# Optimization experiments

Hardware: AMD Instinct MI355X
Metric: run time of the kernel (lower is better)

The kernel has to match this reference:

```python
import jax, jax.numpy as jnp
import numpy as np

P0 = 2   # tublet_size
P = 16   # patch_size
FC = 2   # flow channels (map_x, map_y)


def patchify(x, p0, p1, p2):
    # x: (B, C, T, H, W) -> (B, (T/p0)(H/p1)(W/p2), p0*p1*p2*C)
    B, C, T, H, W = x.shape
    x = x.reshape(B, C, T // p0, p0, H // p1, p1, W // p2, p2)
    x = x.transpose(0, 2, 4, 6, 3, 5, 7, 1)  # b t h w p0 p1 p2 c
    return x.reshape(B, (T // p0) * (H // p1) * (W // p2), p0 * p1 * p2 * C)


def unpatchify(x, p0, p1, p2, C, T, H, W):
    # x: (B, N, p0*p1*p2*C) -> (B, C, T, H, W)
    B = x.shape[0]
    x = x.reshape(B, T // p0, H // p1, W // p2, p0, p1, p2, C)
    x = x.transpose(0, 7, 1, 4, 2, 5, 3, 6)  # b c t p0 h p1 w p2
    return x.reshape(B, C, T, H, W)


def bilinear_warp(imgs, mx, my):
    # imgs: (B, C, T, H, W); mx, my: (B, T, H, W) absolute sample coords.
    # Equivalent of cv2.remap INTER_LINEAR with constant (zero) border.
    B, C, T, H, W = imgs.shape
    x0 = jnp.floor(mx)
    y0 = jnp.floor(my)
    wx = (mx - x0).reshape(B, 1, T, H * W)
    wy = (my - y0).reshape(B, 1, T, H * W)
    x0i = x0.astype(jnp.int32)
    y0i = y0.astype(jnp.int32)
    imgs_flat = imgs.reshape(B, C, T, H * W)

    def gather(yi, xi):
        yc = jnp.clip(yi, 0, H - 1)
        xc = jnp.clip(xi, 0, W - 1)
        idx = (yc * W + xc).reshape(B, 1, T, H * W)
        v = jnp.take_along_axis(imgs_flat, jnp.broadcast_to(idx, (B, C, T, H * W)), axis=-1)
        valid = ((yi >= 0) & (yi <= H - 1) & (xi >= 0) & (xi <= W - 1)).reshape(B, 1, T, H * W)
        return v * valid.astype(v.dtype)

    v00 = gather(y0i, x0i)
    v01 = gather(y0i, x0i + 1)
    v10 = gather(y0i + 1, x0i)
    v11 = gather(y0i + 1, x0i + 1)
    out = (v00 * (1 - wx) * (1 - wy) + v01 * wx * (1 - wy)
           + v10 * (1 - wx) * wy + v11 * wx * wy)
    return out.reshape(B, C, T, H, W)


def setup_inputs() -> dict:
    key = jax.random.key(0)
    k1, k2, k3 = jax.random.split(key, 3)
    B, C, T, H, W = 8, 3, 16, 224, 224
    N = (T // P0) * (H // P) * (W // P)         # 1568 tokens
    D = P0 * P * P * FC                         # 1024 per-token flow dim
    output = jax.random.normal(k1, (B, N, D), dtype=jnp.float32)
    raw_target = jax.random.normal(k2, (B, C, T, H, W), dtype=jnp.float32)
    mask = jax.random.randint(k3, (B, N), 0, 2) > 0
    return {"output": output, "raw_target": raw_target, "mask": mask}


def reference(output, raw_target, mask):
    B, C, T, H, W = raw_target.shape
    # tokens -> dense flow field (B, 2, T, H, W)
    flows = unpatchify(output, P0, P, P, FC, T, H, W)
    gx = jnp.arange(W, dtype=flows.dtype)               # (W,)
    gy = jnp.arange(H, dtype=flows.dtype)[:, None]      # (H, 1)
    mx = flows[:, 0] + gx                                # (B, T, H, W)
    my = flows[:, 1] + gy
    recons = bilinear_warp(raw_target, mx, my)           # (B, C, T, H, W)
    rec_p = patchify(recons, P0, P, P)                   # (B, N, p0*p1*p2*C)
    tgt_p = patchify(raw_target, P0, P, P)
    m = mask.astype(rec_p.dtype)[..., None]              # (B, N, 1)
    diff2 = (rec_p - tgt_p) ** 2 * m
    denom = jnp.maximum(m.sum(), 1.0) * rec_p.shape[-1]
    return diff2.sum() / denom
```

## Files before the change

kernel.cpp:

```cpp
#include <hip/hip_runtime.h>

#define Bd 8
#define Cd 3
#define Td 16
#define Hd 224
#define Wd 224
#define Nd 1568
#define HWd (Hd*Wd)
#define NTOK (Bd*Nd)
#define GRID_MAIN (NTOK*2)
#define PATCH_ELEMS 1536.0

__global__ __launch_bounds__(256, 8)
void flow_mse_gather(const float* __restrict__ outp,
                     const float* __restrict__ raw,
                     const int* __restrict__ mask,
                     float* __restrict__ partial) {
    const int tid = threadIdx.x;
    const int bid = blockIdx.x;
    const int ft  = bid >> 1;
    const int i0  = bid & 1;

    if (mask[ft] == 0) {
        if (tid == 0) partial[bid] = 0.f;
        return;
    }

    const int b  = ft / Nd;
    const int n  = ft - b * Nd;
    const int t2 = n / 196;
    const int rm = n - t2 * 196;
    const int ph = rm / 14;
    const int pw = rm - ph * 14;
    const int t  = (t2 << 1) | i0;

    const int py = tid >> 4, px = tid & 15;
    const int h  = (ph << 4) + py;
    const int w  = (pw << 4) + px;

    const float2 f = ((const float2*)(outp + ((size_t)ft << 10) + (i0 << 9)))[tid];

    const float mx = f.x + (float)w;
    const float my = f.y + (float)h;
    const float x0 = floorf(mx), y0 = floorf(my);
    const float wx = mx - x0,    wy = my - y0;
    const int x0i = (int)x0, y0i = (int)y0;
    const int x1i = x0i + 1,  y1i = y0i + 1;

    const bool vx0 = (x0i >= 0) && (x0i < Wd);
    const bool vx1 = (x1i >= 0) && (x1i < Wd);
    const bool vy0 = (y0i >= 0) && (y0i < Hd);
    const bool vy1 = (y1i >= 0) && (y1i < Hd);

    const float W00 = (1.f - wx) * (1.f - wy) * ((vx0 && vy0) ? 1.f : 0.f);
    const float W01 = wx         * (1.f - wy) * ((vx1 && vy0) ? 1.f : 0.f);
    const float W10 = (1.f - wx) * wy         * ((vx0 && vy1) ? 1.f : 0.f);
    const float W11 = wx         * wy         * ((vx1 && vy1) ? 1.f : 0.f);

    const int xc0 = min(max(x0i, 0), Wd - 1);
    const int xc1 = min(max(x1i, 0), Wd - 1);
    const int yc0 = min(max(y0i, 0), Hd - 1);
    const int yc1 = min(max(y1i, 0), Hd - 1);

    const int i00 = yc0 * Wd + xc0;
    const int i01 = yc0 * Wd + xc1;
    const int i10 = yc1 * Wd + xc0;
    const int i11 = yc1 * Wd + xc1;
    const int itg = h * Wd + w;

    const float* base = raw + (size_t)(b * (Cd * Td) + t) * HWd;
    float acc = 0.f;
    #pragma unroll
    for (int c = 0; c < Cd; ++c) {
        const float* img = base + (size_t)c * (Td * HWd);
        float rec = img[i00] * W00 + img[i01] * W01
                  + img[i10] * W10 + img[i11] * W11;
        float d = rec - img[itg];
        acc += d * d;
    }

    __shared__ float sred[4];
    for (int off = 32; off > 0; off >>= 1) acc += __shfl_down(acc, off, 64);
    if ((tid & 63) == 0) sred[tid >> 6] = acc;
    __syncthreads();
    if (tid == 0) partial[bid] = sred[0] + sred[1] + sred[2] + sred[3];
}

__global__ void finalize_kernel(const float* __restrict__ partial,
                                const int* __restrict__ mask,
                                float* __restrict__ out) {
    const int tid = threadIdx.x;
    double s = 0.0;
    for (int i = tid; i < GRID_MAIN; i += 256) s += (double)partial[i];
    int c = 0;
    for (int i = tid; i < NTOK; i += 256) c += (mask[i] != 0) ? 1 : 0;
    for (int off = 32; off > 0; off >>= 1) {
        s += __shfl_down(s, off, 64);
        c += __shfl_down(c, off, 64);
    }
    __shared__ double sd[4];
    __shared__ int    sc[4];
    int lane = tid & 63, wid = tid >> 6;
    if (lane == 0) { sd[wid] = s; sc[wid] = c; }
    __syncthreads();
    if (tid == 0) {
        double st = sd[0] + sd[1] + sd[2] + sd[3];
        int    ct = sc[0] + sc[1] + sc[2] + sc[3];
        double denom = (double)(ct > 0 ? ct : 1) * PATCH_ELEMS;
        out[0] = (float)(st / denom);
    }
}

extern "C" void kernel_launch(void* const* d_in, const int* in_sizes, int n_in,
                              void* d_out, int out_size, void* d_ws, size_t ws_size,
                              hipStream_t stream) {
    const float* outp = (const float*)d_in[0];
    const float* raw  = (const float*)d_in[1];
    const int*   mask = (const int*)d_in[2];
    float* out = (float*)d_out;

    float* partial = (float*)d_ws;

    flow_mse_gather<<<GRID_MAIN, 256, 0, stream>>>(outp, raw, mask, partial);
    finalize_kernel<<<1, 256, 0, stream>>>(partial, mask, out);
}
```

Before: 190.5 us.

## Compact masked tokens into a list and process both frames per block

A new compaction kernel ballot-scans the mask into a per-segment list of active token indices. The main kernel launches one block per token, and blocks past the active count exit at once, so masked-out tokens no longer occupy blocks that do a mask load before exiting. Each block now handles both temporal frames of a token. Partial sums are combined with a float atomicAdd, which replaces the double-precision finalize pass over partials but makes the summation order nondeterministic and less precise.

```diff
diff --git a/kernel.cpp b/kernel.cpp
--- a/kernel.cpp
+++ b/kernel.cpp
@@ -8,106 +8,154 @@
 #define Nd 1568
 #define HWd (Hd*Wd)
 #define NTOK (Bd*Nd)
-#define GRID_MAIN (NTOK*2)
+#define GRID_MAIN NTOK
+#define NSEG 13
 #define PATCH_ELEMS 1536.0
 
-__global__ __launch_bounds__(256, 8)
+__global__ void compact_kernel(const int* __restrict__ mask,
+                               int* __restrict__ list,
+                               int* __restrict__ bcnt,
+                               float* __restrict__ acc) {
+    const int j   = blockIdx.x;
+    const int tid = threadIdx.x;
+    const int i   = (j << 10) + tid;
+    if (j == 0 && tid == 0) acc[0] = 0.f;
+    bool m = (i < NTOK) && (mask[i] != 0);
+    unsigned long long bal = __ballot(m);
+    int lane = tid & 63, wid = tid >> 6;
+    __shared__ unsigned wt[16];
+    unsigned pre = (unsigned)__popcll(bal & ((1ull << lane) - 1ull));
+    if (lane == 0) wt[wid] = (unsigned)__popcll(bal);
+    __syncthreads();
+    unsigned base = 0;
+    for (int k = 0; k < wid; ++k) base += wt[k];
+    if (m) list[(j << 10) + base + pre] = i;
+    if (tid == 0) {
+        unsigned tot = 0;
+        #pragma unroll
+        for (int k = 0; k < 16; ++k) tot += wt[k];
+        bcnt[j] = (int)tot;
+    }
+}
+
+__global__ __launch_bounds__(256, 6)
 void flow_mse_gather(const float* __restrict__ outp,
                      const float* __restrict__ raw,
-                     const int* __restrict__ mask,
-                     float* __restrict__ partial) {
+                     const int* __restrict__ list,
+                     const int* __restrict__ bcnt,
+                     float* __restrict__ acc) {
     const int tid = threadIdx.x;
     const int bid = blockIdx.x;
-    const int ft  = bid >> 1;
-    const int i0  = bid & 1;
 
-    if (mask[ft] == 0) {
-        if (tid == 0) partial[bid] = 0.f;
-        return;
-    }
+    int pre1  = bcnt[0];
+    int pre2  = pre1  + bcnt[1];
+    int pre3  = pre2  + bcnt[2];
+    int pre4  = pre3  + bcnt[3];
+    int pre5  = pre4  + bcnt[4];
+    int pre6  = pre5  + bcnt[5];
+    int pre7  = pre6  + bcnt[6];
+    int pre8  = pre7  + bcnt[7];
+    int pre9  = pre8  + bcnt[8];
+    int pre10 = pre9  + bcnt[9];
+    int pre11 = pre10 + bcnt[10];
+    int pre12 = pre11 + bcnt[11];
+    const int cnt = pre12 + bcnt[12];
+    if (bid >= cnt) return;
 
-    const int b  = ft / Nd;
-    const int n  = ft - b * Nd;
+    int seg = 0, sbase = 0;
+    if (bid >= pre1)  { seg = 1;  sbase = pre1;  }
+    if (bid >= pre2)  { seg = 2;  sbase = pre2;  }
+    if (bid >= pre3)  { seg = 3;  sbase = pre3;  }
+    if (bid >= pre4)  { seg = 4;  sbase = pre4;  }
+    if (bid >= pre5)  { seg = 5;  sbase = pre5;  }
+    if (bid >= pre6)  { seg = 6;  sbase = pre6;  }
+    if (bid >= pre7)  { seg = 7;  sbase = pre7;  }
+    if (bid >= pre8)  { seg = 8;  sbase = pre8;  }
+    if (bid >= pre9)  { seg = 9;  sbase = pre9;  }
+    if (bid >= pre10) { seg = 10; sbase = pre10; }
+    if (bid >= pre11) { seg = 11; sbase = pre11; }
+    if (bid >= pre12) { seg = 12; sbase = pre12; }
+    const int tk = list[(seg << 10) + bid - sbase];
+
+    const int b  = tk / Nd;
+    const int n  = tk - b * Nd;
     const int t2 = n / 196;
     const int rm = n - t2 * 196;
     const int ph = rm / 14;
     const int pw = rm - ph * 14;
-    const int t  = (t2 << 1) | i0;
 
     const int py = tid >> 4, px = tid & 15;
     const int h  = (ph << 4) + py;
     const int w  = (pw << 4) + px;
-
-    const float2 f = ((const float2*)(outp + ((size_t)ft << 10) + (i0 << 9)))[tid];
-
-    const float mx = f.x + (float)w;
-    const float my = f.y + (float)h;
-    const float x0 = floorf(mx), y0 = floorf(my);
-    const float wx = mx - x0,    wy = my - y0;
-    const int x0i = (int)x0, y0i = (int)y0;
-    const int x1i = x0i + 1,  y1i = y0i + 1;
-
-    const bool vx0 = (x0i >= 0) && (x0i < Wd);
-    const bool vx1 = (x1i >= 0) && (x1i < Wd);
-    const bool vy0 = (y0i >= 0) && (y0i < Hd);
-    const bool vy1 = (y1i >= 0) && (y1i < Hd);
-
-    const float W00 = (1.f - wx) * (1.f - wy) * ((vx0 && vy0) ? 1.f : 0.f);
-    const float W01 = wx         * (1.f - wy) * ((vx1 && vy0) ? 1.f : 0.f);
-    const float W10 = (1.f - wx) * wy         * ((vx0 && vy1) ? 1.f : 0.f);
-    const float W11 = wx         * wy         * ((vx1 && vy1) ? 1.f : 0.f);
-
-    const int xc0 = min(max(x0i, 0), Wd - 1);
-    const int xc1 = min(max(x1i, 0), Wd - 1);
-    const int yc0 = min(max(y0i, 0), Hd - 1);
-    const int yc1 = min(max(y1i, 0), Hd - 1);
-
-    const int i00 = yc0 * Wd + xc0;
-    const int i01 = yc0 * Wd + xc1;
-    const int i10 = yc1 * Wd + xc0;
-    const int i11 = yc1 * Wd + xc1;
     const int itg = h * Wd + w;
 
-    const float* base = raw + (size_t)(b * (Cd * Td) + t) * HWd;
-    float acc = 0.f;
+    const float* frow = outp + ((size_t)tk << 10);
+    float2 f0 = ((const float2*)frow)[tid];
+    float2 f1 = ((const float2*)(frow + 512))[tid];
+
+    float Wt[2][4];
+    int   tp[2][4];
+    #pragma unroll
+    for (int s = 0; s < 2; ++s) {
+        float2 f = s ? f1 : f0;
+        float mx = f.x + (float)w;
+        float my = f.y + (float)h;
+        float x0 = floorf(mx), y0 = floorf(my);
+        float wx = mx - x0,    wy = my - y0;
+        int x0i = (int)x0, y0i = (int)y0;
+        int x1i = x0i + 1,  y1i = y0i + 1;
+
+        bool vx0 = (x0i >= 0) && (x0i < Wd);
+        bool vx1 = (x1i >= 0) && (x1i < Wd);
+        bool vy0 = (y0i >= 0) && (y0i < Hd);
+        bool vy1 = (y1i >= 0) && (y1i < Hd);
+
+        Wt[s][0] = (1.f - wx) * (1.f - wy) * ((vx0 && vy0) ? 1.f : 0.f);
+        Wt[s][1] = wx         * (1.f - wy) * ((vx1 && vy0) ? 1.f : 0.f);
+        Wt[s][2] = (1.f - wx) * wy         * ((vx0 && vy1) ? 1.f : 0.f);
+        Wt[s][3] = wx         * wy         * ((vx1 && vy1) ? 1.f : 0.f);
+
+        int xc0 = min(max(x0i, 0), Wd - 1);
+        int xc1 = min(max(x1i, 0), Wd - 1);
+        int yc0 = min(max(y0i, 0), Hd - 1);
+        int yc1 = min(max(y1i, 0), Hd - 1);
+        tp[s][0] = yc0 * Wd + xc0;
+        tp[s][1] = yc0 * Wd + xc1;
+        tp[s][2] = yc1 * Wd + xc0;
+        tp[s][3] = yc1 * Wd + xc1;
+    }
+
+    float a = 0.f;
     #pragma unroll
     for (int c = 0; c < Cd; ++c) {
-        const float* img = base + (size_t)c * (Td * HWd);
-        float rec = img[i00] * W00 + img[i01] * W01
-                  + img[i10] * W10 + img[i11] * W11;
-        float d = rec - img[itg];
-        acc += d * d;
+        #pragma unroll
+        for (int s = 0; s < 2; ++s) {
+            const float* img = raw
+                + (size_t)((b * Cd + c) * Td + (t2 << 1) + s) * HWd;
+            float rec = img[tp[s][0]] * Wt[s][0] + img[tp[s][1]] * Wt[s][1]
+                      + img[tp[s][2]] * Wt[s][2] + img[tp[s][3]] * Wt[s][3];
+            float d = rec - img[itg];
+            a += d * d;
+        }
     }
 
     __shared__ float sred[4];
-    for (int off = 32; off > 0; off >>= 1) acc += __shfl_down(acc, off, 64);
-    if ((tid & 63) == 0) sred[tid >> 6] = acc;
+    for (int off = 32; off > 0; off >>= 1) a += __shfl_down(a, off, 64);
+    if ((tid & 63) == 0) sred[tid >> 6] = a;
     __syncthreads();
-    if (tid == 0) partial[bid] = sred[0] + sred[1] + sred[2] + sred[3];
+    if (tid == 0)
+        atomicAdd(acc, sred[0] + sred[1] + sred[2] + sred[3]);
 }
 
-__global__ void finalize_kernel(const float* __restrict__ partial,
-                                const int* __restrict__ mask,
+__global__ void finalize_kernel(const float* __restrict__ acc,
+                                const int* __restrict__ bcnt,
                                 float* __restrict__ out) {
-    const int tid = threadIdx.x;
-    double s = 0.0;
-    for (int i = tid; i < GRID_MAIN; i += 256) s += (double)partial[i];
-    int c = 0;
-    for (int i = tid; i < NTOK; i += 256) c += (mask[i] != 0) ? 1 : 0;
-    for (int off = 32; off > 0; off >>= 1) {
-        s += __shfl_down(s, off, 64);
-        c += __shfl_down(c, off, 64);
-    }
-    __shared__ double sd[4];
-    __shared__ int    sc[4];
-    int lane = tid & 63, wid = tid >> 6;
-    if (lane == 0) { sd[wid] = s; sc[wid] = c; }
-    __syncthreads();
-    if (tid == 0) {
-        double st = sd[0] + sd[1] + sd[2] + sd[3];
-        int    ct = sc[0] + sc[1] + sc[2] + sc[3];
+    if (threadIdx.x == 0) {
+        int ct = 0;
+        #pragma unroll
+        for (int k = 0; k < NSEG; ++k) ct += bcnt[k];
         double denom = (double)(ct > 0 ? ct : 1) * PATCH_ELEMS;
-        out[0] = (float)(st / denom);
+        out[0] = (float)((double)acc[0] / denom);
     }
 }
 
@@ -119,8 +167,11 @@
     const int*   mask = (const int*)d_in[2];
     float* out = (float*)d_out;
 
-    float* partial = (float*)d_ws;
+    float* acc  = (float*)d_ws;
+    int*   bcnt = (int*)((char*)d_ws + 64);
+    int*   list = (int*)((char*)d_ws + 128);
 
-    flow_mse_gather<<<GRID_MAIN, 256, 0, stream>>>(outp, raw, mask, partial);
-    finalize_kernel<<<1, 256, 0, stream>>>(partial, mask, out);
+    compact_kernel<<<NSEG, 1024, 0, stream>>>(mask, list, bcnt, acc);
+    flow_mse_gather<<<GRID_MAIN, 256, 0, stream>>>(outp, raw, list, bcnt, acc);
+    finalize_kernel<<<1, 64, 0, stream>>>(acc, bcnt, out);
 }
```

After: 204.4 us. 1.07x slower.

## Stage halo row strips in LDS with a prefetching persistent gather kernel

Applied to the files above, without the earlier changes.

Replaces the one-block-per-token gather kernel with a persistent kernel. Each work item loads a 20-row strip of one image plane (16 rows plus a 2-row halo) into LDS with float4 loads, and the bilinear samples for all masked patches in that strip are read from LDS. The loop falls back to global memory only when a sample lands outside the halo. The next strip is prefetched into registers while the current one is computed, and work items are ordered by XCD. Mask counts per strip and an atomicAdd of the partial sums replace the partial-sum array. The accumulation into the output is never zeroed inside the launch, so results depend on the output buffer being cleared beforehand.

```diff
diff --git a/kernel.cpp b/kernel.cpp
--- a/kernel.cpp
+++ b/kernel.cpp
@@ -7,107 +7,184 @@
 #define Wd 224
 #define Nd 1568
 #define HWd (Hd*Wd)
-#define NTOK (Bd*Nd)
-#define GRID_MAIN (NTOK*2)
+#define NPH 14
+#define NPW 14
+#define NT2 8
+#define NSTRIP (Bd*NT2*NPH)
+#define NUNIT (NSTRIP*2)
+#define NITEM (NUNIT*3)
+#define UPX (NUNIT/8)
+#define GRID_MAIN 2048
+#define HALO 2
+#define SROWS 20
+#define LROW Wd
+#define LDS_FLOATS (SROWS*LROW)
+#define STG_GRAN (SROWS*56)
 #define PATCH_ELEMS 1536.0
 
-__global__ __launch_bounds__(256, 8)
-void flow_mse_gather(const float* __restrict__ outp,
-                     const float* __restrict__ raw,
-                     const int* __restrict__ mask,
-                     float* __restrict__ partial) {
-    const int tid = threadIdx.x;
-    const int bid = blockIdx.x;
-    const int ft  = bid >> 1;
-    const int i0  = bid & 1;
-
-    if (mask[ft] == 0) {
-        if (tid == 0) partial[bid] = 0.f;
-        return;
+struct Geo {
+    const float* plane;
+    int b, i0, c, strip, ph, ybase, nbase;
+};
+
+__device__ __forceinline__ Geo decode(int it, const float* __restrict__ raw) {
+    Geo g;
+    const int xcd  = it & 7;
+    const int slot = it >> 3;
+    g.c    = slot % 3;
+    const int ul = slot / 3;
+    const int u  = xcd * UPX + ul;
+    g.strip = u >> 1;
+    g.i0    = u & 1;
+    g.b     = g.strip / (NT2 * NPH);
+    const int sr = g.strip - g.b * (NT2 * NPH);
+    const int t2 = sr / NPH;
+    g.ph    = sr - t2 * NPH;
+    g.ybase = (g.ph << 4) - HALO;
+    g.nbase = t2 * 196 + g.ph * NPW;
+    const int t = (t2 << 1) | g.i0;
+    g.plane = raw + ((size_t)(g.b * Cd + g.c) * Td + t) * HWd;
+    return g;
+}
+
+#define ROWLOAD(G, V, DST) do {                                          \
+    const int _v = (V);                                                  \
+    const int _j = _v / 56, _c4 = _v - _j * 56;                          \
+    const int _yc = min(max((G).ybase + _j, 0), Hd - 1);                 \
+    DST = *(const float4*)((G).plane + _yc * Wd + (_c4 << 2));           \
+} while (0)
+
+#define ISSUE(G) do {                                                    \
+    ROWLOAD(G, tid,        r0);                                          \
+    ROWLOAD(G, tid + 256,  r1);                                          \
+    ROWLOAD(G, tid + 512,  r2);                                          \
+    ROWLOAD(G, tid + 768,  r3);                                          \
+    if (tid < STG_GRAN - 1024) ROWLOAD(G, tid + 1024, r4);               \
+} while (0)
+
+__global__ __launch_bounds__(256, 4)
+void flow_mse_pipe(const float* __restrict__ outp,
+                   const float* __restrict__ raw,
+                   const int* __restrict__ mask,
+                   int* __restrict__ scnt,
+                   float* __restrict__ out) {
+    __shared__ float lds[LDS_FLOATS];
+    __shared__ float sred[4];
+    const int tid  = threadIdx.x;
+    const int lane = tid & 63;
+    const int py = tid >> 4, px = tid & 15;
+
+    float acc = 0.f;
+
+    int item = (int)blockIdx.x;
+    Geo g = decode(item, raw);
+    float4 r0, r1, r2, r3, r4;
+    ISSUE(g);
+
+    while (item < NITEM) {
+        const int nitem = item + GRID_MAIN;
+
+        *(float4*)(lds + (tid << 2))         = r0;
+        *(float4*)(lds + ((tid + 256) << 2)) = r1;
+        *(float4*)(lds + ((tid + 512) << 2)) = r2;
+        *(float4*)(lds + ((tid + 768) << 2)) = r3;
+        if (tid < STG_GRAN - 1024) *(float4*)(lds + ((tid + 1024) << 2)) = r4;
+
+        bool mm = (lane < NPW) && (mask[g.b * Nd + g.nbase + lane] != 0);
+        unsigned mw = (unsigned)(__ballot(mm) & 0x3FFFull);
+        if (g.c == 0 && g.i0 == 0 && tid == 0) scnt[g.strip] = __popc(mw);
+
+        int pw = 0;
+        float2 f = make_float2(0.f, 0.f);
+        if (mw) {
+            pw = __ffs((int)mw) - 1;
+            f = ((const float2*)(outp + ((size_t)(g.b * Nd + g.nbase + pw) << 10)
+                                 + (g.i0 << 9)))[tid];
+        }
+
+        __syncthreads();
+
+        Geo gn;
+        const bool have = nitem < NITEM;
+        if (have) { gn = decode(nitem, raw); ISSUE(gn); }
+
+        const int h = (g.ph << 4) + py;
+        while (mw) {
+            const unsigned nmw = mw & (mw - 1);
+            int npw = 0;
+            float2 nf = make_float2(0.f, 0.f);
+            if (nmw) {
+                npw = __ffs((int)nmw) - 1;
+                nf = ((const float2*)(outp
+                        + ((size_t)(g.b * Nd + g.nbase + npw) << 10)
+                        + (g.i0 << 9)))[tid];
+            }
+
+            const int w  = (pw << 4) + px;
+            const float mx = f.x + (float)w;
+            const float my = f.y + (float)h;
+            const float x0 = floorf(mx), y0 = floorf(my);
+            const float wx = mx - x0,    wy = my - y0;
+            const int x0i = (int)x0, y0i = (int)y0;
+            const int x1i = x0i + 1,  y1i = y0i + 1;
+
+            const bool vx0 = (x0i >= 0) && (x0i < Wd);
+            const bool vx1 = (x1i >= 0) && (x1i < Wd);
+            const bool vy0 = (y0i >= 0) && (y0i < Hd);
+            const bool vy1 = (y1i >= 0) && (y1i < Hd);
+
+            const float W00 = (1.f - wx) * (1.f - wy) * ((vx0 && vy0) ? 1.f : 0.f);
+            const float W01 = wx         * (1.f - wy) * ((vx1 && vy0) ? 1.f : 0.f);
+            const float W10 = (1.f - wx) * wy         * ((vx0 && vy1) ? 1.f : 0.f);
+            const float W11 = wx         * wy         * ((vx1 && vy1) ? 1.f : 0.f);
+
+            const int xc0 = min(max(x0i, 0), Wd - 1);
+            const int xc1 = min(max(x1i, 0), Wd - 1);
+            const int yc0 = min(max(y0i, 0), Hd - 1);
+            const int yc1 = min(max(y1i, 0), Hd - 1);
+            const int ly0 = yc0 - g.ybase, ly1 = yc1 - g.ybase;
+
+            const float tg = lds[(py + HALO) * LROW + w];
+            float rec;
+            if ((ly0 >= 0) & (ly1 < SROWS)) {
+                rec = lds[ly0 * LROW + xc0] * W00 + lds[ly0 * LROW + xc1] * W01
+                    + lds[ly1 * LROW + xc0] * W10 + lds[ly1 * LROW + xc1] * W11;
+            } else {
+                rec = g.plane[yc0 * Wd + xc0] * W00 + g.plane[yc0 * Wd + xc1] * W01
+                    + g.plane[yc1 * Wd + xc0] * W10 + g.plane[yc1 * Wd + xc1] * W11;
+            }
+            const float d = rec - tg;
+            acc += d * d;
+
+            mw = nmw; pw = npw; f = nf;
+        }
+
+        __syncthreads();
+        item = nitem;
+        if (have) g = gn;
     }
 
-    const int b  = ft / Nd;
-    const int n  = ft - b * Nd;
-    const int t2 = n / 196;
-    const int rm = n - t2 * 196;
-    const int ph = rm / 14;
-    const int pw = rm - ph * 14;
-    const int t  = (t2 << 1) | i0;
-
-    const int py = tid >> 4, px = tid & 15;
-    const int h  = (ph << 4) + py;
-    const int w  = (pw << 4) + px;
-
-    const float2 f = ((const float2*)(outp + ((size_t)ft << 10) + (i0 << 9)))[tid];
-
-    const float mx = f.x + (float)w;
-    const float my = f.y + (float)h;
-    const float x0 = floorf(mx), y0 = floorf(my);
-    const float wx = mx - x0,    wy = my - y0;
-    const int x0i = (int)x0, y0i = (int)y0;
-    const int x1i = x0i + 1,  y1i = y0i + 1;
-
-    const bool vx0 = (x0i >= 0) && (x0i < Wd);
-    const bool vx1 = (x1i >= 0) && (x1i < Wd);
-    const bool vy0 = (y0i >= 0) && (y0i < Hd);
-    const bool vy1 = (y1i >= 0) && (y1i < Hd);
-
-    const float W00 = (1.f - wx) * (1.f - wy) * ((vx0 && vy0) ? 1.f : 0.f);
-    const float W01 = wx         * (1.f - wy) * ((vx1 && vy0) ? 1.f : 0.f);
-    const float W10 = (1.f - wx) * wy         * ((vx0 && vy1) ? 1.f : 0.f);
-    const float W11 = wx         * wy         * ((vx1 && vy1) ? 1.f : 0.f);
-
-    const int xc0 = min(max(x0i, 0), Wd - 1);
-    const int xc1 = min(max(x1i, 0), Wd - 1);
-    const int yc0 = min(max(y0i, 0), Hd - 1);
-    const int yc1 = min(max(y1i, 0), Hd - 1);
-
-    const int i00 = yc0 * Wd + xc0;
-    const int i01 = yc0 * Wd + xc1;
-    const int i10 = yc1 * Wd + xc0;
-    const int i11 = yc1 * Wd + xc1;
-    const int itg = h * Wd + w;
-
-    const float* base = raw + (size_t)(b * (Cd * Td) + t) * HWd;
-    float acc = 0.f;
-    #pragma unroll
-    for (int c = 0; c < Cd; ++c) {
-        const float* img = base + (size_t)c * (Td * HWd);
-        float rec = img[i00] * W00 + img[i01] * W01
-                  + img[i10] * W10 + img[i11] * W11;
-        float d = rec - img[itg];
-        acc += d * d;
-    }
-
-    __shared__ float sred[4];
     for (int off = 32; off > 0; off >>= 1) acc += __shfl_down(acc, off, 64);
-    if ((tid & 63) == 0) sred[tid >> 6] = acc;
+    if (lane == 0) sred[tid >> 6] = acc;
     __syncthreads();
-    if (tid == 0) partial[bid] = sred[0] + sred[1] + sred[2] + sred[3];
-}
-
-__global__ void finalize_kernel(const float* __restrict__ partial,
-                                const int* __restrict__ mask,
+    if (tid == 0)
+        atomicAdd(out, sred[0] + sred[1] + sred[2] + sred[3]);
+}
+
+__global__ void finalize_kernel(const int* __restrict__ scnt,
                                 float* __restrict__ out) {
     const int tid = threadIdx.x;
-    double s = 0.0;
-    for (int i = tid; i < GRID_MAIN; i += 256) s += (double)partial[i];
-    int c = 0;
-    for (int i = tid; i < NTOK; i += 256) c += (mask[i] != 0) ? 1 : 0;
-    for (int off = 32; off > 0; off >>= 1) {
-        s += __shfl_down(s, off, 64);
-        c += __shfl_down(c, off, 64);
-    }
-    __shared__ double sd[4];
-    __shared__ int    sc[4];
-    int lane = tid & 63, wid = tid >> 6;
-    if (lane == 0) { sd[wid] = s; sc[wid] = c; }
+    int c = scnt[tid] + scnt[tid + 256] + scnt[tid + 512];
+    if (tid < NSTRIP - 768) c += scnt[tid + 768];
+    for (int off = 32; off > 0; off >>= 1) c += __shfl_down(c, off, 64);
+    __shared__ int sc[4];
+    const int lane = tid & 63, wid = tid >> 6;
+    if (lane == 0) sc[wid] = c;
     __syncthreads();
     if (tid == 0) {
-        double st = sd[0] + sd[1] + sd[2] + sd[3];
-        int    ct = sc[0] + sc[1] + sc[2] + sc[3];
-        double denom = (double)(ct > 0 ? ct : 1) * PATCH_ELEMS;
-        out[0] = (float)(st / denom);
+        const int ct = sc[0] + sc[1] + sc[2] + sc[3];
+        const double denom = (double)(ct > 0 ? ct : 1) * PATCH_ELEMS;
+        out[0] = (float)((double)out[0] / denom);
     }
 }
 
@@ -119,8 +196,8 @@
     const int*   mask = (const int*)d_in[2];
     float* out = (float*)d_out;
 
-    float* partial = (float*)d_ws;
-
-    flow_mse_gather<<<GRID_MAIN, 256, 0, stream>>>(outp, raw, mask, partial);
-    finalize_kernel<<<1, 256, 0, stream>>>(partial, mask, out);
-}
+    int* scnt = (int*)d_ws;
+
+    flow_mse_pipe<<<GRID_MAIN, 256, 0, stream>>>(outp, raw, mask, scnt, out);
+    finalize_kernel<<<1, 256, 0, stream>>>(scnt, out);
+}
```

Result: faster. 169.0 us (-11.3%).
